# Performance work log

Hardware: AMD Instinct MI355X
Metric: run time of the kernel (lower is better)

The kernel has to match this reference:

```python
import jax, jax.numpy as jnp
from jax import lax
import numpy as np

BATCH = 128
SEQ = 80
EMB = 100
VOCAB = 10000
UNITS = 2048


def setup_inputs() -> dict:
    key = jax.random.key(0)
    ks = jax.random.split(key, 10)
    s_in = 1.0 / np.sqrt(EMB)
    s_u = 1.0 / np.sqrt(UNITS)
    return {
        "tokens": jax.random.randint(ks[0], (BATCH, SEQ), 0, VOCAB, dtype=jnp.int32),
        "emb": jax.random.normal(ks[1], (VOCAB, EMB), dtype=jnp.float32) * 0.05,
        # layer 0: input dim EMB -> UNITS
        "W0": jax.random.normal(ks[2], (EMB, UNITS), dtype=jnp.float32) * s_in,
        "U0": jax.random.normal(ks[3], (UNITS, UNITS), dtype=jnp.float32) * s_u,
        "b0": jnp.zeros((UNITS,), dtype=jnp.float32),
        # shared cell (source bug: rnn_cell1 reused for layers 1, 2 and 3)
        "W1": jax.random.normal(ks[4], (UNITS, UNITS), dtype=jnp.float32) * s_u,
        "U1": jax.random.normal(ks[5], (UNITS, UNITS), dtype=jnp.float32) * s_u,
        "b1": jnp.zeros((UNITS,), dtype=jnp.float32),
        # output head
        "Wo": jax.random.normal(ks[6], (UNITS, 1), dtype=jnp.float32) * s_u,
        "bo": jnp.zeros((1,), dtype=jnp.float32),
    }


def reference(tokens, emb, W0, U0, b0, W1, U1, b1, Wo, bo):
    x = emb[tokens]  # [B, T, E]
    B = x.shape[0]
    U = W0.shape[1]

    def step(carry, xt):
        h0, h1, h2, h3 = carry
        # SimpleRNNCell: h' = tanh(x @ W + h @ U + b); inference (no dropout)
        h0 = jnp.tanh(xt @ W0 + h0 @ U0 + b0)
        h1 = jnp.tanh(h0 @ W1 + h1 @ U1 + b1)  # layers 1-3 share W1/U1/b1
        h2 = jnp.tanh(h1 @ W1 + h2 @ U1 + b1)
        h3 = jnp.tanh(h2 @ W1 + h3 @ U1 + b1)
        return (h0, h1, h2, h3), None

    init = tuple(jnp.zeros((B, U), x.dtype) for _ in range(4))
    (_, _, _, h3), _ = lax.scan(step, init, jnp.swapaxes(x, 0, 1))  # scan over time
    return jax.nn.sigmoid(h3 @ Wo + bo)  # [B, 1]
```

## Files before the change

kernel.cpp:

```cpp
#include <hip/hip_runtime.h>
#include <hip/hip_bf16.h>

#define BATCH 128
#define SEQ   80
#define EMB   100
#define UNITS 2048

typedef __attribute__((ext_vector_type(8))) short bf16x8;
typedef __attribute__((ext_vector_type(4))) float f32x4;

static __device__ __forceinline__ short f2bf(float f) {
  __hip_bfloat16 h = __float2bfloat16(f);
  return *reinterpret_cast<short*>(&h);
}
static __device__ __forceinline__ float bf2f(short s) {
  __hip_bfloat16 h = *reinterpret_cast<__hip_bfloat16*>(&s);
  return __bfloat162float(h);
}


__global__ __launch_bounds__(256) void pack_b_kernel(
    const float* __restrict__ src, int Ksrc, int N, int nch, int totalUnits,
    short* __restrict__ dst) {
  int lane = threadIdx.x & 63;
  int u = blockIdx.x * 4 + (threadIdx.x >> 6);
  if (u >= totalUnits) return;
  int c  = u / nch;
  int kk = u - c * nch;
  int n  = c * 16 + (lane & 15);
  int k0 = kk * 32 + ((lane >> 4) << 3);
  bf16x8 v;
#pragma unroll
  for (int j = 0; j < 8; ++j) {
    int k = k0 + j;
    float f = (k < Ksrc) ? src[k * N + n] : 0.f;
    v[j] = f2bf(f);
  }
  *reinterpret_cast<bf16x8*>(dst + (u * 64 + lane) * 8) = v;
}

__global__ __launch_bounds__(256) void pack_e_kernel(
    const int* __restrict__ tokens, const float* __restrict__ emb,
    short* __restrict__ Ep2) {
  int idx = blockIdx.x * 256 + threadIdx.x;
  if (idx >= SEQ * 8 * 8 * 64) return;
  int lane = idx & 63;
  int kq = (idx >> 6) & 7;
  int r  = (idx >> 9) & 7;
  int t  = idx >> 12;
  int b  = r * 16 + (lane & 15);
  int k0 = kq * 32 + ((lane >> 4) << 3);
  int tok = tokens[b * SEQ + t];
  bf16x8 v;
#pragma unroll
  for (int j = 0; j < 8; ++j) {
    int k = k0 + j;
    v[j] = (k < EMB) ? f2bf(emb[tok * EMB + k]) : (short)0;
  }
  *reinterpret_cast<bf16x8*>(Ep2 + (size_t)idx * 8) = v;
}

#define MFMA(a, b, c) __builtin_amdgcn_mfma_f32_16x16x32_bf16((a), (b), (c), 0, 0, 0)

static __device__ __forceinline__ void gload16(const void* g, void* l) {
  __builtin_amdgcn_global_load_lds(
      (const __attribute__((address_space(1))) void*)g,
      (__attribute__((address_space(3))) void*)l, 16, 0, 0);
}

struct BF { bf16x8 v[4]; };

#define WAITV(N) asm volatile("s_waitcnt vmcnt(" #N ")" ::: "memory")

__global__ __launch_bounds__(512) void diag_kernel(
    const short* __restrict__ Ep2,
    const short* __restrict__ W0p, const short* __restrict__ U0p,
    const short* __restrict__ Wsp, const short* __restrict__ Usp,
    const float* __restrict__ b0, const float* __restrict__ b1,
    short* __restrict__ hbase, int s) {
  __shared__ char lds[131072];

  const int tid  = threadIdx.x;
  const int lane = tid & 63;
  const int w    = tid >> 6;

  int bid = blockIdx.x;
  int xcd = bid & 7, idx = bid >> 3;
  int cb  = xcd * 4 + (idx & 3);
  int rb  = idx >> 2;
  int l   = rb >> 1;
  int t   = s - l;
  if (t < 0 || t >= SEQ) return;

  const size_t hsz = (size_t)8 * 64 * 64 * 8;
  const int pw = s & 1, pr = pw ^ 1;
  auto hb = [&](int ll, int p) { return hbase + (size_t)(ll * 2 + p) * hsz; };

  const char *Aseg0, *Aseg1, *Bseg0, *Bseg1;
  size_t aStr0;
  int bNch0;
  int steps0, total;
  if (l == 0) {
    Aseg0 = (const char*)(Ep2 + (size_t)t * 32768); aStr0 = 8192;
    Bseg0 = (const char*)W0p; bNch0 = 8;
    Aseg1 = (const char*)hb(0, pr);
    Bseg1 = (const char*)U0p;
    steps0 = 1; total = 9;
  } else {
    Aseg0 = (const char*)hb(l - 1, pr); aStr0 = 65536;
    Bseg0 = (const char*)Wsp; bNch0 = 64;
    Aseg1 = (const char*)hb(l, pr);
    Bseg1 = (const char*)Usp;
    steps0 = 8; total = 16;
  }
  const int rloc0 = (rb & 1) * 4;
  const int ct0   = cb * 4;
  const size_t lb16 = (size_t)lane * 16;

  char* dstT = &lds[0] + (size_t)w * 1024 + lb16;
  auto issueA = [&](int g) {
    char* dst = dstT + (size_t)(g & 3) * 32768;
    const char* src;
    size_t rstr;
    if (g < steps0) {
      src = Aseg0 + (size_t)rloc0 * aStr0 + (size_t)(g * 8 + w) * 1024 + lb16;
      rstr = aStr0;
    } else {
      src = Aseg1 + (size_t)rloc0 * 65536 + (size_t)((g - steps0) * 8 + w) * 1024 + lb16;
      rstr = 65536;
    }
#pragma unroll
    for (int j = 0; j < 4; ++j)
      gload16(src + j * rstr, dst + j * 8192);
  };

#define LOADB(BN, GS)                                                         \
  do {                                                                        \
    const int gs_ = (GS);                                                     \
    const char* base_; size_t nch_; int kq_;                                  \
    if (gs_ < steps0) { base_ = Bseg0; nch_ = bNch0; kq_ = gs_ * 8 + w; }     \
    else { base_ = Bseg1; nch_ = 64; kq_ = (gs_ - steps0) * 8 + w; }          \
    _Pragma("unroll")                                                         \
    for (int i = 0; i < 4; ++i) {                                             \
      const char* p_ = base_ + ((size_t)(ct0 + i) * nch_ + kq_) * 1024 + lb16; \
      asm volatile("global_load_dwordx4 %0, %1, off" : "=v"(BN.v[i]) : "v"(p_)); \
    }                                                                         \
  } while (0)

  f32x4 acc[4][4];
#pragma unroll
  for (int r = 0; r < 4; ++r)
#pragma unroll
    for (int c = 0; c < 4; ++c) acc[r][c] = (f32x4){0.f, 0.f, 0.f, 0.f};

  auto computeStep = [&](int g, const BF& Bf) {
    const char* base = &lds[0] + (size_t)(g & 3) * 32768;
#pragma unroll
    for (int r = 0; r < 4; ++r) {
      bf16x8 av = *(const bf16x8*)(base + (size_t)r * 8192 + (size_t)w * 1024 + lb16);
#pragma unroll
      for (int c = 0; c < 4; ++c)
        acc[r][c] = MFMA(av, Bf.v[c], acc[r][c]);
    }
  };

#define STEP(G, BCUR, BNXT)                                          \
  do {                                                               \
    const int g_ = (G);                                              \
    if (g_ + 1 < total) LOADB(BNXT, g_ + 1);                         \
    if (g_ + 2 < total) issueA(g_ + 2);                              \
    if (g_ + 2 < total) { WAITV(12); }                               \
    else if (g_ + 1 < total) { WAITV(8); }                           \
    else { WAITV(0); }                                               \
    __builtin_amdgcn_s_barrier();                                    \
    __builtin_amdgcn_sched_barrier(0);                               \
    computeStep(g_, BCUR);                                           \
    __builtin_amdgcn_sched_barrier(0);                               \
  } while (0)

  BF Bq0, Bq1;
  issueA(0); LOADB(Bq0, 0); issueA(1);

  for (int g = 0; g < total; g += 2) {
    STEP(g, Bq0, Bq1);
    if (g + 1 < total) STEP(g + 1, Bq1, Bq0);
  }
#undef STEP
#undef LOADB

  __syncthreads();
  {
    char* dst = &lds[0] + (size_t)w * 16384;
#pragma unroll
    for (int r = 0; r < 4; ++r)
#pragma unroll
      for (int c = 0; c < 4; ++c)
        *(f32x4*)(dst + (((size_t)(r * 4 + c) * 64 + lane) << 4)) = acc[r][c];
  }
  __syncthreads();

  const float* bias = (l == 0) ? b0 : b1;
  short* H = hb(l, pw);
  const int lo = lane & 15, hi = lane >> 4;
  const int mb = (rb & 1) * 64;
#pragma unroll
  for (int cc = 0; cc < 2; ++cc) {
    const int cell = w * 2 + cc;
    const int r = cell >> 2, c = cell & 3;
    const size_t coff = (((size_t)cell * 64 + lane) << 4);
    f32x4 sum = *(const f32x4*)(&lds[0] + coff);
#pragma unroll
    for (int p = 1; p < 8; ++p)
      sum += *(const f32x4*)(&lds[0] + (size_t)p * 16384 + coff);
    const int n = cb * 64 + c * 16 + lo;
    const float bv = bias[n];
    const int kk = n >> 5;
    const int lpn = ((n >> 3) & 3) << 4;
#pragma unroll
    for (int i = 0; i < 4; ++i) {
      int m = mb + r * 16 + hi * 4 + i;
      float z = sum[i] + bv;
      float e = __expf(2.f * z);
      float th = 1.f - 2.f / (e + 1.f);
      int rr = m >> 4;
      int lp = (m & 15) | lpn;
      H[(((size_t)rr * 64 + kk) * 64 + lp) * 8 + (n & 7)] = f2bf(th);
    }
  }
}

__global__ __launch_bounds__(256) void head_kernel(
    const short* __restrict__ h3, const float* __restrict__ Wo,
    const float* __restrict__ bo, float* __restrict__ out) {
  __shared__ float sred[4];
  int b = blockIdx.x, tid = threadIdx.x;
  int kk = tid >> 2, hi = tid & 3;
  const bf16x8 v = *reinterpret_cast<const bf16x8*>(
      h3 + (((size_t)(b >> 4) * 64 + kk) * 64 + ((b & 15) | (hi << 4))) * 8);
  int k0 = kk * 32 + hi * 8;
  float acc = 0.f;
#pragma unroll
  for (int j = 0; j < 8; ++j) acc += bf2f(v[j]) * Wo[k0 + j];
  for (int off = 32; off > 0; off >>= 1) acc += __shfl_down(acc, off);
  if ((tid & 63) == 0) sred[tid >> 6] = acc;
  __syncthreads();
  if (tid == 0) {
    float z = sred[0] + sred[1] + sred[2] + sred[3] + bo[0];
    out[b] = 1.f / (1.f + expf(-z));
  }
}

extern "C" void kernel_launch(void* const* d_in, const int* in_sizes, int n_in,
                              void* d_out, int out_size, void* d_ws, size_t ws_size,
                              hipStream_t stream) {
  const int*   tokens = (const int*)d_in[0];
  const float* emb    = (const float*)d_in[1];
  const float* W0     = (const float*)d_in[2];
  const float* U0     = (const float*)d_in[3];
  const float* b0     = (const float*)d_in[4];
  const float* W1     = (const float*)d_in[5];
  const float* U1     = (const float*)d_in[6];
  const float* b1     = (const float*)d_in[7];
  const float* Wo     = (const float*)d_in[8];
  const float* bo     = (const float*)d_in[9];
  float* out = (float*)d_out;
  short* ws  = (short*)d_ws;

  const size_t W0P_SZ = (size_t)128 * 8 * 512;
  const size_t UP_SZ  = (size_t)128 * 64 * 512;
  const size_t EP_SZ  = (size_t)SEQ * 32768;
  const size_t H_SZ   = (size_t)8 * 64 * 64 * 8;

  short* W0p = ws;
  short* U0p = W0p + W0P_SZ;
  short* W1p = U0p + UP_SZ;
  short* U1p = W1p + UP_SZ;
  short* Ep2 = U1p + UP_SZ;
  short* hbase = Ep2 + EP_SZ;

  {
    int unitsW0 = (UNITS / 16) * 8;
    pack_b_kernel<<<(unitsW0 + 3) / 4, 256, 0, stream>>>(W0, EMB, UNITS, 8, unitsW0, W0p);
    int unitsU = (UNITS / 16) * (UNITS / 32);
    pack_b_kernel<<<(unitsU + 3) / 4, 256, 0, stream>>>(U0, UNITS, UNITS, UNITS / 32, unitsU, U0p);
    pack_b_kernel<<<(unitsU + 3) / 4, 256, 0, stream>>>(W1, UNITS, UNITS, UNITS / 32, unitsU, W1p);
    pack_b_kernel<<<(unitsU + 3) / 4, 256, 0, stream>>>(U1, UNITS, UNITS, UNITS / 32, unitsU, U1p);
    int ne = SEQ * 8 * 8 * 64;
    pack_e_kernel<<<(ne + 255) / 256, 256, 0, stream>>>(tokens, emb, Ep2);
  }

  hipMemsetAsync(hbase, 0, 8u * H_SZ * 2u, stream);

  for (int s = 0; s <= SEQ - 1 + 3; ++s) {
    diag_kernel<<<256, 512, 0, stream>>>(Ep2, W0p, U0p, W1p, U1p, b0, b1, hbase, s);
  }

  head_kernel<<<BATCH, 256, 0, stream>>>(hbase + 6 * H_SZ, Wo, bo, out);
}
```

Before: 1.340 ms.

## Split batch rows finer and partition waves by N and K in diagonal kernel

```diff
diff --git a/kernel.cpp b/kernel.cpp
--- a/kernel.cpp
+++ b/kernel.cpp
@@ -68,7 +68,7 @@
       (__attribute__((address_space(3))) void*)l, 16, 0, 0);
 }
 
-struct BF { bf16x8 v[4]; };
+struct BF { bf16x8 v[2][2]; };
 
 #define WAITV(N) asm volatile("s_waitcnt vmcnt(" #N ")" ::: "memory")
 
@@ -78,18 +78,20 @@
     const short* __restrict__ Wsp, const short* __restrict__ Usp,
     const float* __restrict__ b0, const float* __restrict__ b1,
     short* __restrict__ hbase, int s) {
-  __shared__ char lds[131072];
+  __shared__ char lds[65536];
 
   const int tid  = threadIdx.x;
   const int lane = tid & 63;
   const int w    = tid >> 6;
+  const int wc = w & 1, wk = w >> 1;
 
   int bid = blockIdx.x;
   int xcd = bid & 7, idx = bid >> 3;
-  int cb  = xcd * 4 + (idx & 3);
-  int rb  = idx >> 2;
-  int l   = rb >> 1;
-  int t   = s - l;
+  int cb   = xcd * 4 + (idx & 3);
+  int rem2 = idx >> 2;
+  int rs   = rem2 & 3;
+  int l    = rem2 >> 2;
+  int t    = s - l;
   if (t < 0 || t >= SEQ) return;
 
   const size_t hsz = (size_t)8 * 64 * 64 * 8;
@@ -97,70 +99,79 @@
   auto hb = [&](int ll, int p) { return hbase + (size_t)(ll * 2 + p) * hsz; };
 
   const char *Aseg0, *Aseg1, *Bseg0, *Bseg1;
-  size_t aStr0;
-  int bNch0;
+  size_t aRow0;
+  int nchB0;
   int steps0, total;
   if (l == 0) {
-    Aseg0 = (const char*)(Ep2 + (size_t)t * 32768); aStr0 = 8192;
-    Bseg0 = (const char*)W0p; bNch0 = 8;
+    Aseg0 = (const char*)(Ep2 + (size_t)t * 32768); aRow0 = 8192;
+    Bseg0 = (const char*)W0p; nchB0 = 8;
     Aseg1 = (const char*)hb(0, pr);
     Bseg1 = (const char*)U0p;
     steps0 = 1; total = 9;
   } else {
-    Aseg0 = (const char*)hb(l - 1, pr); aStr0 = 65536;
-    Bseg0 = (const char*)Wsp; bNch0 = 64;
+    Aseg0 = (const char*)hb(l - 1, pr); aRow0 = 65536;
+    Bseg0 = (const char*)Wsp; nchB0 = 64;
     Aseg1 = (const char*)hb(l, pr);
     Bseg1 = (const char*)Usp;
     steps0 = 8; total = 16;
   }
-  const int rloc0 = (rb & 1) * 4;
-  const int ct0   = cb * 4;
+  const int rt0 = rs * 2;
   const size_t lb16 = (size_t)lane * 16;
 
-  char* dstT = &lds[0] + (size_t)w * 1024 + lb16;
+  const int uA = tid >> 6;
+  const char* a0T = Aseg0 + (size_t)rt0 * aRow0 + (size_t)uA * 1024 + lb16;
+  const char* a1T = Aseg1 + (size_t)rt0 * 65536 + (size_t)uA * 1024 + lb16;
+  char* dT = &lds[0] + (size_t)uA * 1024 + lb16;
+
   auto issueA = [&](int g) {
-    char* dst = dstT + (size_t)(g & 3) * 32768;
-    const char* src;
-    size_t rstr;
-    if (g < steps0) {
-      src = Aseg0 + (size_t)rloc0 * aStr0 + (size_t)(g * 8 + w) * 1024 + lb16;
-      rstr = aStr0;
-    } else {
-      src = Aseg1 + (size_t)rloc0 * 65536 + (size_t)((g - steps0) * 8 + w) * 1024 + lb16;
-      rstr = 65536;
-    }
-#pragma unroll
-    for (int j = 0; j < 4; ++j)
-      gload16(src + j * rstr, dst + j * 8192);
+    char* dst = dT + (size_t)(g & 3) * 16384;
+    const char* src; size_t xstr;
+    if (g < steps0) { src = a0T + (size_t)g * 8192; xstr = aRow0; }
+    else            { src = a1T + (size_t)(g - steps0) * 8192; xstr = 65536; }
+    gload16(src, dst);
+    gload16(src + xstr, dst + 8192);
   };
+
+  const char* bS0[2], *bS1[2];
+  bS0[0] = Bseg0 + ((size_t)(cb * 4 + wc * 2 + 0) * nchB0 + wk * 2) * 1024 + lb16;
+  bS0[1] = Bseg0 + ((size_t)(cb * 4 + wc * 2 + 1) * nchB0 + wk * 2) * 1024 + lb16;
+  bS1[0] = Bseg1 + ((size_t)(cb * 4 + wc * 2 + 0) * 64 + wk * 2) * 1024 + lb16;
+  bS1[1] = Bseg1 + ((size_t)(cb * 4 + wc * 2 + 1) * 64 + wk * 2) * 1024 + lb16;
 
 #define LOADB(BN, GS)                                                         \
   do {                                                                        \
     const int gs_ = (GS);                                                     \
-    const char* base_; size_t nch_; int kq_;                                  \
-    if (gs_ < steps0) { base_ = Bseg0; nch_ = bNch0; kq_ = gs_ * 8 + w; }     \
-    else { base_ = Bseg1; nch_ = 64; kq_ = (gs_ - steps0) * 8 + w; }          \
-    _Pragma("unroll")                                                         \
-    for (int i = 0; i < 4; ++i) {                                             \
-      const char* p_ = base_ + ((size_t)(ct0 + i) * nch_ + kq_) * 1024 + lb16; \
-      asm volatile("global_load_dwordx4 %0, %1, off" : "=v"(BN.v[i]) : "v"(p_)); \
+    const char *p0_, *p1_;                                                    \
+    if (gs_ < steps0) {                                                       \
+      size_t o_ = (size_t)gs_ * 8192;                                         \
+      p0_ = bS0[0] + o_; p1_ = bS0[1] + o_;                                   \
+    } else {                                                                  \
+      size_t o_ = (size_t)(gs_ - steps0) * 8192;                              \
+      p0_ = bS1[0] + o_; p1_ = bS1[1] + o_;                                   \
     }                                                                         \
+    asm volatile("global_load_dwordx4 %0, %1, off" : "=v"(BN.v[0][0]) : "v"(p0_));        \
+    asm volatile("global_load_dwordx4 %0, %1, off" : "=v"(BN.v[0][1]) : "v"(p0_ + 1024)); \
+    asm volatile("global_load_dwordx4 %0, %1, off" : "=v"(BN.v[1][0]) : "v"(p1_));        \
+    asm volatile("global_load_dwordx4 %0, %1, off" : "=v"(BN.v[1][1]) : "v"(p1_ + 1024)); \
   } while (0)
 
-  f32x4 acc[4][4];
-#pragma unroll
-  for (int r = 0; r < 4; ++r)
-#pragma unroll
-    for (int c = 0; c < 4; ++c) acc[r][c] = (f32x4){0.f, 0.f, 0.f, 0.f};
+  f32x4 acc[2][2];
+#pragma unroll
+  for (int x = 0; x < 2; ++x)
+#pragma unroll
+    for (int y = 0; y < 2; ++y) acc[x][y] = (f32x4){0.f, 0.f, 0.f, 0.f};
 
   auto computeStep = [&](int g, const BF& Bf) {
-    const char* base = &lds[0] + (size_t)(g & 3) * 32768;
-#pragma unroll
-    for (int r = 0; r < 4; ++r) {
-      bf16x8 av = *(const bf16x8*)(base + (size_t)r * 8192 + (size_t)w * 1024 + lb16);
-#pragma unroll
-      for (int c = 0; c < 4; ++c)
-        acc[r][c] = MFMA(av, Bf.v[c], acc[r][c]);
+    const char* base = &lds[0] + (size_t)(g & 3) * 16384;
+#pragma unroll
+    for (int x = 0; x < 2; ++x) {
+      bf16x8 av0 = *(const bf16x8*)(base + (((x * 8 + wk * 2 + 0) << 10) + lb16));
+      bf16x8 av1 = *(const bf16x8*)(base + (((x * 8 + wk * 2 + 1) << 10) + lb16));
+#pragma unroll
+      for (int y = 0; y < 2; ++y) {
+        acc[x][y] = MFMA(av0, Bf.v[y][0], acc[x][y]);
+        acc[x][y] = MFMA(av1, Bf.v[y][1], acc[x][y]);
+      }
     }
   };
 
@@ -169,8 +180,8 @@
     const int g_ = (G);                                              \
     if (g_ + 1 < total) LOADB(BNXT, g_ + 1);                         \
     if (g_ + 2 < total) issueA(g_ + 2);                              \
-    if (g_ + 2 < total) { WAITV(12); }                               \
-    else if (g_ + 1 < total) { WAITV(8); }                           \
+    if (g_ + 2 < total) { WAITV(8); }                                \
+    else if (g_ + 1 < total) { WAITV(6); }                           \
     else { WAITV(0); }                                               \
     __builtin_amdgcn_s_barrier();                                    \
     __builtin_amdgcn_sched_barrier(0);                               \
@@ -189,44 +200,49 @@
 #undef LOADB
 
   __syncthreads();
-  {
-    char* dst = &lds[0] + (size_t)w * 16384;
-#pragma unroll
-    for (int r = 0; r < 4; ++r)
-#pragma unroll
-      for (int c = 0; c < 4; ++c)
-        *(f32x4*)(dst + (((size_t)(r * 4 + c) * 64 + lane) << 4)) = acc[r][c];
+  if (wk != 0) {
+    char* d = &lds[0] + ((size_t)((wk - 1) * 2 + wc) << 12);
+#pragma unroll
+    for (int x = 0; x < 2; ++x)
+#pragma unroll
+      for (int y = 0; y < 2; ++y)
+        *(f32x4*)(d + (((x * 2 + y) << 10) + lb16)) = acc[x][y];
   }
   __syncthreads();
+  if (wk != 0) return;
+#pragma unroll
+  for (int p = 0; p < 3; ++p) {
+    const char* sp = &lds[0] + ((size_t)(p * 2 + wc) << 12);
+#pragma unroll
+    for (int x = 0; x < 2; ++x)
+#pragma unroll
+      for (int y = 0; y < 2; ++y)
+        acc[x][y] += *(const f32x4*)(sp + (((x * 2 + y) << 10) + lb16));
+  }
 
   const float* bias = (l == 0) ? b0 : b1;
   short* H = hb(l, pw);
   const int lo = lane & 15, hi = lane >> 4;
-  const int mb = (rb & 1) * 64;
-#pragma unroll
-  for (int cc = 0; cc < 2; ++cc) {
-    const int cell = w * 2 + cc;
-    const int r = cell >> 2, c = cell & 3;
-    const size_t coff = (((size_t)cell * 64 + lane) << 4);
-    f32x4 sum = *(const f32x4*)(&lds[0] + coff);
-#pragma unroll
-    for (int p = 1; p < 8; ++p)
-      sum += *(const f32x4*)(&lds[0] + (size_t)p * 16384 + coff);
-    const int n = cb * 64 + c * 16 + lo;
-    const float bv = bias[n];
-    const int kk = n >> 5;
-    const int lpn = ((n >> 3) & 3) << 4;
-#pragma unroll
-    for (int i = 0; i < 4; ++i) {
-      int m = mb + r * 16 + hi * 4 + i;
-      float z = sum[i] + bv;
-      float e = __expf(2.f * z);
-      float th = 1.f - 2.f / (e + 1.f);
-      int rr = m >> 4;
-      int lp = (m & 15) | lpn;
-      H[(((size_t)rr * 64 + kk) * 64 + lp) * 8 + (n & 7)] = f2bf(th);
+  const int nb = cb * 64 + wc * 32;
+  const float bv0 = bias[nb + lo];
+  const float bv1 = bias[nb + 16 + lo];
+#pragma unroll
+  for (int x = 0; x < 2; ++x)
+#pragma unroll
+    for (int y = 0; y < 2; ++y) {
+      float bbv = y ? bv1 : bv0;
+#pragma unroll
+      for (int i = 0; i < 4; ++i) {
+        int m = rs * 32 + x * 16 + hi * 4 + i;
+        int n = nb + y * 16 + lo;
+        float z = acc[x][y][i] + bbv;
+        float e = __expf(2.f * z);
+        float th = 1.f - 2.f / (e + 1.f);
+        int rr = m >> 4, kk = n >> 5;
+        int lp = (m & 15) | (((n >> 3) & 3) << 4);
+        H[(((size_t)rr * 64 + kk) * 64 + lp) * 8 + (n & 7)] = f2bf(th);
+      }
     }
-  }
 }
 
 __global__ __launch_bounds__(256) void head_kernel(
@@ -292,7 +308,7 @@
   hipMemsetAsync(hbase, 0, 8u * H_SZ * 2u, stream);
 
   for (int s = 0; s <= SEQ - 1 + 3; ++s) {
-    diag_kernel<<<256, 512, 0, stream>>>(Ep2, W0p, U0p, W1p, U1p, b0, b1, hbase, s);
+    diag_kernel<<<512, 512, 0, stream>>>(Ep2, W0p, U0p, W1p, U1p, b0, b1, hbase, s);
   }
 
   head_kernel<<<BATCH, 256, 0, stream>>>(hbase + 6 * H_SZ, Wo, bo, out);
```

Result: slower. 1.519 ms (+13.3%).

## Load A tiles straight into registers with triple-buffered prefetch, drop LDS staging

Applied to the files above, without the earlier changes.

```diff
diff --git a/kernel.cpp b/kernel.cpp
--- a/kernel.cpp
+++ b/kernel.cpp
@@ -62,13 +62,7 @@
 
 #define MFMA(a, b, c) __builtin_amdgcn_mfma_f32_16x16x32_bf16((a), (b), (c), 0, 0, 0)
 
-static __device__ __forceinline__ void gload16(const void* g, void* l) {
-  __builtin_amdgcn_global_load_lds(
-      (const __attribute__((address_space(1))) void*)g,
-      (__attribute__((address_space(3))) void*)l, 16, 0, 0);
-}
-
-struct BF { bf16x8 v[4]; };
+struct FR { bf16x8 a[4]; bf16x8 b[4]; };
 
 #define WAITV(N) asm volatile("s_waitcnt vmcnt(" #N ")" ::: "memory")
 
@@ -98,17 +92,17 @@
 
   const char *Aseg0, *Aseg1, *Bseg0, *Bseg1;
   size_t aStr0;
-  int bNch0;
+  int nchB0;
   int steps0, total;
   if (l == 0) {
     Aseg0 = (const char*)(Ep2 + (size_t)t * 32768); aStr0 = 8192;
-    Bseg0 = (const char*)W0p; bNch0 = 8;
+    Bseg0 = (const char*)W0p; nchB0 = 8;
     Aseg1 = (const char*)hb(0, pr);
     Bseg1 = (const char*)U0p;
     steps0 = 1; total = 9;
   } else {
     Aseg0 = (const char*)hb(l - 1, pr); aStr0 = 65536;
-    Bseg0 = (const char*)Wsp; bNch0 = 64;
+    Bseg0 = (const char*)Wsp; nchB0 = 64;
     Aseg1 = (const char*)hb(l, pr);
     Bseg1 = (const char*)Usp;
     steps0 = 8; total = 16;
@@ -117,33 +111,39 @@
   const int ct0   = cb * 4;
   const size_t lb16 = (size_t)lane * 16;
 
-  char* dstT = &lds[0] + (size_t)w * 1024 + lb16;
-  auto issueA = [&](int g) {
-    char* dst = dstT + (size_t)(g & 3) * 32768;
-    const char* src;
-    size_t rstr;
-    if (g < steps0) {
-      src = Aseg0 + (size_t)rloc0 * aStr0 + (size_t)(g * 8 + w) * 1024 + lb16;
-      rstr = aStr0;
-    } else {
-      src = Aseg1 + (size_t)rloc0 * 65536 + (size_t)((g - steps0) * 8 + w) * 1024 + lb16;
-      rstr = 65536;
-    }
-#pragma unroll
-    for (int j = 0; j < 4; ++j)
-      gload16(src + j * rstr, dst + j * 8192);
-  };
-
-#define LOADB(BN, GS)                                                         \
+  const char* a0B = Aseg0 + (size_t)rloc0 * aStr0 + (size_t)w * 1024 + lb16;
+  const char* a1B = Aseg1 + (size_t)rloc0 * 65536 + (size_t)w * 1024 + lb16;
+  const char* b0B[4];
+  const char* b1B[4];
+#pragma unroll
+  for (int ct = 0; ct < 4; ++ct) {
+    b0B[ct] = Bseg0 + ((size_t)(ct0 + ct) * nchB0 + w) * 1024 + lb16;
+    b1B[ct] = Bseg1 + ((size_t)(ct0 + ct) * 64 + w) * 1024 + lb16;
+  }
+
+#define LOADSET(SN, GS)                                                       \
   do {                                                                        \
     const int gs_ = (GS);                                                     \
-    const char* base_; size_t nch_; int kq_;                                  \
-    if (gs_ < steps0) { base_ = Bseg0; nch_ = bNch0; kq_ = gs_ * 8 + w; }     \
-    else { base_ = Bseg1; nch_ = 64; kq_ = (gs_ - steps0) * 8 + w; }          \
-    _Pragma("unroll")                                                         \
-    for (int i = 0; i < 4; ++i) {                                             \
-      const char* p_ = base_ + ((size_t)(ct0 + i) * nch_ + kq_) * 1024 + lb16; \
-      asm volatile("global_load_dwordx4 %0, %1, off" : "=v"(BN.v[i]) : "v"(p_)); \
+    if (gs_ < steps0) {                                                       \
+      size_t o_ = (size_t)gs_ * 8192;                                         \
+      _Pragma("unroll")                                                       \
+      for (int rt = 0; rt < 4; ++rt)                                          \
+        asm volatile("global_load_dwordx4 %0, %1, off"                        \
+                     : "=v"(SN.a[rt]) : "v"(a0B + (size_t)rt * aStr0 + o_));  \
+      _Pragma("unroll")                                                       \
+      for (int ct = 0; ct < 4; ++ct)                                          \
+        asm volatile("global_load_dwordx4 %0, %1, off"                        \
+                     : "=v"(SN.b[ct]) : "v"(b0B[ct] + o_));                   \
+    } else {                                                                  \
+      size_t o_ = (size_t)(gs_ - steps0) * 8192;                              \
+      _Pragma("unroll")                                                       \
+      for (int rt = 0; rt < 4; ++rt)                                          \
+        asm volatile("global_load_dwordx4 %0, %1, off"                        \
+                     : "=v"(SN.a[rt]) : "v"(a1B + (size_t)rt * 65536 + o_));  \
+      _Pragma("unroll")                                                       \
+      for (int ct = 0; ct < 4; ++ct)                                          \
+        asm volatile("global_load_dwordx4 %0, %1, off"                        \
+                     : "=v"(SN.b[ct]) : "v"(b1B[ct] + o_));                   \
     }                                                                         \
   } while (0)
 
@@ -153,40 +153,35 @@
 #pragma unroll
     for (int c = 0; c < 4; ++c) acc[r][c] = (f32x4){0.f, 0.f, 0.f, 0.f};
 
-  auto computeStep = [&](int g, const BF& Bf) {
-    const char* base = &lds[0] + (size_t)(g & 3) * 32768;
-#pragma unroll
-    for (int r = 0; r < 4; ++r) {
-      bf16x8 av = *(const bf16x8*)(base + (size_t)r * 8192 + (size_t)w * 1024 + lb16);
-#pragma unroll
-      for (int c = 0; c < 4; ++c)
-        acc[r][c] = MFMA(av, Bf.v[c], acc[r][c]);
-    }
-  };
-
-#define STEP(G, BCUR, BNXT)                                          \
+#define STEP(G, CUR, NX2)                                            \
   do {                                                               \
     const int g_ = (G);                                              \
-    if (g_ + 1 < total) LOADB(BNXT, g_ + 1);                         \
-    if (g_ + 2 < total) issueA(g_ + 2);                              \
-    if (g_ + 2 < total) { WAITV(12); }                               \
+    if (g_ + 2 < total) { LOADSET(NX2, g_ + 2); WAITV(16); }         \
     else if (g_ + 1 < total) { WAITV(8); }                           \
     else { WAITV(0); }                                               \
-    __builtin_amdgcn_s_barrier();                                    \
     __builtin_amdgcn_sched_barrier(0);                               \
-    computeStep(g_, BCUR);                                           \
+    _Pragma("unroll")                                                \
+    for (int rt = 0; rt < 4; ++rt)                                   \
+      _Pragma("unroll")                                              \
+      for (int ct = 0; ct < 4; ++ct)                                 \
+        acc[rt][ct] = MFMA(CUR.a[rt], CUR.b[ct], acc[rt][ct]);       \
     __builtin_amdgcn_sched_barrier(0);                               \
   } while (0)
 
-  BF Bq0, Bq1;
-  issueA(0); LOADB(Bq0, 0); issueA(1);
-
-  for (int g = 0; g < total; g += 2) {
-    STEP(g, Bq0, Bq1);
-    if (g + 1 < total) STEP(g + 1, Bq1, Bq0);
-  }
+  FR S0, S1, S2;
+  LOADSET(S0, 0);
+  LOADSET(S1, 1);
+
+  int g = 0;
+  for (; g + 3 <= total; g += 3) {
+    STEP(g,     S0, S2);
+    STEP(g + 1, S1, S0);
+    STEP(g + 2, S2, S1);
+  }
+  if (g < total) { STEP(g, S0, S2); ++g; }
+  if (g < total) { STEP(g, S1, S0); ++g; }
 #undef STEP
-#undef LOADB
+#undef LOADSET
 
   __syncthreads();
   {
```

Measured after the change: 1.186 ms. 1.13x faster.
